# Optimization experiments

Hardware: AMD Instinct MI355X
Metric: run time of the kernel (lower is better)

Reference implementation:

```python
import jax, jax.numpy as jnp
import numpy as np

D_MODEL = 1024
N_EXPERTS = 16
TOP_K = 2
EXPERT_DIM = 1024
SHARED_DIM = 2048
B, T = 2, 1024


def setup_inputs() -> dict:
    key = jax.random.key(0)
    ks = jax.random.split(key, 7)
    std = 0.02
    return {
        "x": jax.random.normal(ks[0], (B, T, D_MODEL), dtype=jnp.float32),
        "router_w": jax.random.normal(ks[1], (N_EXPERTS, D_MODEL), dtype=jnp.float32) * std,
        "gate_up_w": jax.random.normal(ks[2], (N_EXPERTS, D_MODEL, 2 * EXPERT_DIM), dtype=jnp.float32) * std,
        "down_w": jax.random.normal(ks[3], (N_EXPERTS, EXPERT_DIM, D_MODEL), dtype=jnp.float32) * std,
        "shared_gate_w": jax.random.normal(ks[4], (SHARED_DIM, D_MODEL), dtype=jnp.float32) * std,
        "shared_up_w": jax.random.normal(ks[5], (SHARED_DIM, D_MODEL), dtype=jnp.float32) * std,
        "shared_down_w": jax.random.normal(ks[6], (D_MODEL, SHARED_DIM), dtype=jnp.float32) * std,
    }


def reference(x, router_w, gate_up_w, down_w, shared_gate_w, shared_up_w, shared_down_w):
    Bb, Tt, C = x.shape
    N = Bb * Tt
    E = gate_up_w.shape[0]

    # Router: top-k logits, sigmoid gating (matches torch.topk then sigmoid).
    logits = jnp.einsum('btc,ec->bte', x, router_w)          # [B,T,E]
    top_vals, top_idx = jax.lax.top_k(logits, TOP_K)          # [B,T,K]
    gates = jax.nn.sigmoid(top_vals)

    xf = x.reshape(N, C)
    sel = top_idx.reshape(N, TOP_K)
    gw = gates.reshape(N, TOP_K)

    # Dense per-token expert gate [N,E]: zero except selected experts.
    # top_k indices are distinct per token, so scatter-add == scatter-set.
    w_full = jnp.zeros((N, E), dtype=x.dtype).at[jnp.arange(N)[:, None], sel].add(gw)

    # Run every token through every expert densely (same math as the
    # per-token gather + bmm + scatter_add combine, without materializing
    # [N*K, C, 2H] gathered weight tensors).
    gu = jnp.einsum('nc,ech->neh', xf, gate_up_w)             # [N,E,2H]
    gate, up = jnp.split(gu, 2, axis=-1)
    h = jax.nn.silu(gate) * up                                # [N,E,H]
    out_all = jnp.einsum('neh,ehc->nec', h, down_w)           # [N,E,C]
    moe = jnp.einsum('ne,nec->nc', w_full, out_all).reshape(Bb, Tt, C)

    # Shared expert (SwiGLU MLP).
    sg = jnp.einsum('btc,sc->bts', x, shared_gate_w)
    su = jnp.einsum('btc,sc->bts', x, shared_up_w)
    shared = jnp.einsum('bts,cs->btc', jax.nn.silu(sg) * su, shared_down_w)

    return moe + shared
```

## Files before the change

kernel.cpp:

```cpp
#include <hip/hip_runtime.h>
#include <cstdint>

#define N_TOK 2048
#define CDIM  1024
#define NEXP  16
#define TOPK  2
#define HDIM  1024
#define SDIM  2048
#define ESLOT 48
#define ESLOT64 80
#define GU_EXP_BLOCKS (ESLOT * 16)
#define GU_SH_BLOCKS  (16 * 32)
#define GU_NWG (GU_EXP_BLOCKS + GU_SH_BLOCKS)
#define DN_EXP_BLOCKS (ESLOT64 * 8)
#define DN_SH_BLOCKS  (32 * 8)
#define DN_NWG (DN_EXP_BLOCKS + DN_SH_BLOCKS)

typedef __bf16 bf16;
typedef __bf16 bf16x8 __attribute__((ext_vector_type(8)));
typedef float  f32x4  __attribute__((ext_vector_type(4)));
typedef unsigned int u32;
typedef unsigned short u16;

typedef __attribute__((address_space(3))) uint32_t lds_u32_t;
typedef __attribute__((address_space(1))) uint32_t glb_u32_t;

__device__ __forceinline__ void gload16(const void* g, void* l) {
  __builtin_amdgcn_global_load_lds((const glb_u32_t*)(uintptr_t)g,
                                   (lds_u32_t*)(uintptr_t)l, 16, 0, 0);
}
__device__ __forceinline__ float fromb(u16 s) {
  union { float f; u32 u; } z; z.u = ((u32)s) << 16; return z.f;
}
__device__ __forceinline__ int xcd_swz(int bid, int nwg) {
  return (bid & 7) * (nwg >> 3) + (bid >> 3);
}
#define SBAR0() __builtin_amdgcn_sched_barrier(0)
#define WAIT_VM(N) do { asm volatile("s_waitcnt vmcnt(" #N ")" ::: "memory"); \
                        SBAR0(); } while (0)

__global__ void convert_plain(const float* __restrict__ s, bf16* __restrict__ d) {
  int i = (blockIdx.x * 256 + threadIdx.x) * 8;
  float4 f0 = *(const float4*)(s + i);
  float4 f1 = *(const float4*)(s + i + 4);
  bf16x8 v;
  v[0]=(bf16)f0.x; v[1]=(bf16)f0.y; v[2]=(bf16)f0.z; v[3]=(bf16)f0.w;
  v[4]=(bf16)f1.x; v[5]=(bf16)f1.y; v[6]=(bf16)f1.z; v[7]=(bf16)f1.w;
  *(bf16x8*)(d + i) = v;
}

__global__ __launch_bounds__(256)
void convert_t(const float* __restrict__ src, bf16* __restrict__ dst, int K, int N) {
  __shared__ float ld[64 * 68];
  const int e = blockIdx.z;
  const int n0 = blockIdx.x * 64, k0 = blockIdx.y * 64;
  const float* s = src + (size_t)e * K * N;
  bf16* d = dst + (size_t)e * N * K;
  const int t = threadIdx.x;
  const int kk = t >> 4, c4 = (t & 15) * 4;
#pragma unroll
  for (int q = 0; q < 4; ++q) {
    float4 f = *(const float4*)(s + (size_t)(k0 + kk + q * 16) * N + n0 + c4);
    float* lp = &ld[(kk + q * 16) * 68 + c4];
    lp[0] = f.x; lp[1] = f.y; lp[2] = f.z; lp[3] = f.w;
  }
  __syncthreads();
  const int nn = t >> 2, kc = (t & 3) * 16;
  bf16x8 v0, v1;
#pragma unroll
  for (int j = 0; j < 8; ++j) {
    v0[j] = (bf16)ld[(kc + j) * 68 + nn];
    v1[j] = (bf16)ld[(kc + 8 + j) * 68 + nn];
  }
  bf16* dp = d + (size_t)(n0 + nn) * K + k0 + kc;
  *(bf16x8*)dp = v0;
  *(bf16x8*)(dp + 8) = v1;
}

__global__ void router_kernel(const float* __restrict__ x,
                              const float* __restrict__ rw,
                              bf16* __restrict__ xb,
                              int* __restrict__ sel,
                              float* __restrict__ gatew) {
  int n = blockIdx.x;
  int lane = threadIdx.x;
  const float* xr = x + (size_t)n * CDIM;
  float xv[16];
#pragma unroll
  for (int q = 0; q < 4; ++q) {
    float4 f = *(const float4*)(xr + lane * 16 + q * 4);
    xv[q * 4 + 0] = f.x; xv[q * 4 + 1] = f.y; xv[q * 4 + 2] = f.z; xv[q * 4 + 3] = f.w;
  }
  bf16x8 v0, v1;
#pragma unroll
  for (int j = 0; j < 8; ++j) { v0[j] = (bf16)xv[j]; v1[j] = (bf16)xv[8 + j]; }
  bf16* xo = xb + (size_t)n * CDIM + lane * 16;
  *(bf16x8*)xo = v0;
  *(bf16x8*)(xo + 8) = v1;
  float acc[NEXP];
#pragma unroll
  for (int e = 0; e < NEXP; ++e) {
    float a = 0.f;
    const float* rwe = rw + e * CDIM + lane * 16;
#pragma unroll
    for (int j = 0; j < 16; ++j) a += xv[j] * rwe[j];
    acc[e] = a;
  }
#pragma unroll
  for (int off = 32; off > 0; off >>= 1) {
#pragma unroll
    for (int e = 0; e < NEXP; ++e) acc[e] += __shfl_xor(acc[e], off, 64);
  }
  if (lane == 0) {
    int i0 = 0; float v0_ = acc[0];
#pragma unroll
    for (int e = 1; e < NEXP; ++e) if (acc[e] > v0_) { v0_ = acc[e]; i0 = e; }
    int i1 = (i0 == 0) ? 1 : 0; float v1_ = acc[i1];
#pragma unroll
    for (int e = 0; e < NEXP; ++e) if (e != i0 && acc[e] > v1_) { v1_ = acc[e]; i1 = e; }
    sel[2 * n] = i0; sel[2 * n + 1] = i1;
    gatew[2 * n]     = 1.f / (1.f + expf(-v0_));
    gatew[2 * n + 1] = 1.f / (1.f + expf(-v1_));
  }
}

__global__ void scan_kernel(const int* __restrict__ sel,
                            int* __restrict__ counts,
                            int* __restrict__ offsets,
                            int* __restrict__ cursor,
                            int* __restrict__ tab128,
                            int* __restrict__ tab64,
                            int* __restrict__ ntiles) {
  __shared__ int hist[NEXP];
  const int t = threadIdx.x;
  if (t < NEXP) hist[t] = 0;
  __syncthreads();
  for (int i = t; i < N_TOK * TOPK; i += 256) atomicAdd(&hist[sel[i]], 1);
  __syncthreads();
  if (t == 0) {
    int s = 0, a = 0, b = 0;
    for (int e = 0; e < NEXP; ++e) {
      int c = hist[e];
      counts[e] = c; offsets[e] = s; cursor[e] = s;
      for (int m0 = 0; m0 < c; m0 += 128) tab128[a++] = (e << 16) | m0;
      for (int m0 = 0; m0 < c; m0 += 64)  tab64[b++]  = (e << 16) | m0;
      s += c;
    }
    ntiles[0] = a; ntiles[1] = b;
  }
}

__global__ void scatter_kernel(const int* __restrict__ sel,
                               const float* __restrict__ gatew,
                               int* __restrict__ cursor,
                               int* __restrict__ entry_token,
                               float* __restrict__ entry_gate,
                               int* __restrict__ entry_pos) {
  int t = blockIdx.x * blockDim.x + threadIdx.x;
  if (t >= N_TOK * TOPK) return;
  int e = sel[t];
  int pos = atomicAdd(&cursor[e], 1);
  entry_token[pos] = t >> 1;
  entry_gate[pos] = gatew[t];
  entry_pos[t] = pos;
}

__global__ __launch_bounds__(256, 2)
void gu7(const bf16* __restrict__ xb,
         const bf16* __restrict__ guwb,
         const bf16* __restrict__ sgwb,
         const bf16* __restrict__ suwb,
         bf16* __restrict__ h_exp,
         bf16* __restrict__ h_sh,
         const int* __restrict__ counts,
         const int* __restrict__ offsets,
         const int* __restrict__ entry_token,
         const int* __restrict__ tab128,
         const int* __restrict__ ntiles) {
  __shared__ __align__(16) bf16 sA[2 * 8192];
  __shared__ __align__(16) bf16 sBg[3 * 4096];
  __shared__ __align__(16) bf16 sBu[3 * 4096];

  const int bid = xcd_swz(blockIdx.x, GU_NWG);
  const int t = threadIdx.x;
  const bool is_exp = bid < GU_EXP_BLOCKS;
  const int wid = t >> 6, lane = t & 63;

  int n0, mguard;
  bf16* hbase; int hstride;
  const bf16 *Bg, *Bu;
  const int srow = t >> 3;
  const int sc = (t & 7) ^ (srow & 7);
  const bf16* asrc[4];

  if (is_exp) {
    const int slot = bid >> 4;
    if (slot >= ntiles[0]) return;
    const int packed = tab128[slot];
    const int e = packed >> 16;
    const int m0 = packed & 0xffff;
    const int cnt = counts[e];
    const int base = offsets[e];
    n0 = (bid & 15) * 64;
    mguard = cnt - m0;
#pragma unroll
    for (int i = 0; i < 4; ++i) {
      int r = m0 + i * 32 + srow;
      int tok = entry_token[base + ((r < cnt) ? r : (cnt - 1))];
      asrc[i] = xb + (size_t)tok * CDIM + sc * 8;
    }
    const bf16* we = guwb + (size_t)e * (2 * HDIM) * CDIM;
    Bg = we + (size_t)n0 * CDIM;
    Bu = we + (size_t)(HDIM + n0) * CDIM;
    hbase = h_exp + (size_t)(base + m0) * HDIM + n0;
    hstride = HDIM;
  } else {
    const int sid = bid - GU_EXP_BLOCKS;
    const int m0 = (sid >> 5) * 128;
    n0 = (sid & 31) * 64;
    mguard = 128;
#pragma unroll
    for (int i = 0; i < 4; ++i)
      asrc[i] = xb + (size_t)(m0 + i * 32 + srow) * CDIM + sc * 8;
    Bg = sgwb + (size_t)n0 * CDIM;
    Bu = suwb + (size_t)n0 * CDIM;
    hbase = h_sh + (size_t)m0 * SDIM + n0;
    hstride = SDIM;
  }

  const bf16* bg0 = Bg + (size_t)srow * CDIM + sc * 8;
  const bf16* bu0 = Bu + (size_t)srow * CDIM + sc * 8;
  const int adst = t * 8;

#define ISSUE_A(k_, ab_)                                                      \
  do {                                                                        \
    _Pragma("unroll")                                                         \
    for (int i = 0; i < 4; ++i)                                               \
      gload16(asrc[i] + (k_), &sA[(ab_) * 8192 + adst + i * 2048]);           \
  } while (0)
#define ISSUE_B(k_, bo_)                                                      \
  do {                                                                        \
    _Pragma("unroll")                                                         \
    for (int i = 0; i < 2; ++i) {                                             \
      gload16(bg0 + (size_t)i * 32 * CDIM + (k_), &sBg[(bo_) + adst + i * 2048]); \
      gload16(bu0 + (size_t)i * 32 * CDIM + (k_), &sBu[(bo_) + adst + i * 2048]); \
    }                                                                         \
  } while (0)

  const int wr = (wid >> 1) * 64, wc = (wid & 1) * 32;
  const int lrow = lane & 15, grp = lane >> 4;

  f32x4 ag[4][2], au[4][2];
#pragma unroll
  for (int m = 0; m < 4; ++m)
#pragma unroll
    for (int n = 0; n < 2; ++n)
#pragma unroll
      for (int i = 0; i < 4; ++i) { ag[m][n][i] = 0.f; au[m][n][i] = 0.f; }

#define COMPUTE(ab_, bo_)                                                     \
  do {                                                                        \
    _Pragma("unroll")                                                         \
    for (int ks = 0; ks < 2; ++ks) {                                          \
      const int ch = ks * 4 + grp;                                            \
      bf16x8 av[4], bg[2], bu[2];                                             \
      _Pragma("unroll")                                                       \
      for (int m = 0; m < 4; ++m) {                                           \
        const int r = wr + m * 16 + lrow;                                     \
        av[m] = *(const bf16x8*)&sA[(ab_) * 8192 + r * 64 + ((ch ^ (r & 7)) << 3)]; \
      }                                                                       \
      _Pragma("unroll")                                                       \
      for (int n = 0; n < 2; ++n) {                                           \
        const int r = wc + n * 16 + lrow;                                     \
        bg[n] = *(const bf16x8*)&sBg[(bo_) + r * 64 + ((ch ^ (r & 7)) << 3)]; \
        bu[n] = *(const bf16x8*)&sBu[(bo_) + r * 64 + ((ch ^ (r & 7)) << 3)]; \
      }                                                                       \
      _Pragma("unroll")                                                       \
      for (int m = 0; m < 4; ++m)                                             \
        _Pragma("unroll")                                                     \
        for (int n = 0; n < 2; ++n) {                                         \
          ag[m][n] = __builtin_amdgcn_mfma_f32_16x16x32_bf16(av[m], bg[n], ag[m][n], 0, 0, 0); \
          au[m][n] = __builtin_amdgcn_mfma_f32_16x16x32_bf16(av[m], bu[n], au[m][n], 0, 0, 0); \
        }                                                                     \
    }                                                                         \
  } while (0)

  ISSUE_A(0, 0);
  ISSUE_B(0, 0);
  SBAR0();
  ISSUE_B(64, 4096);
  SBAR0();
  WAIT_VM(4);
  __builtin_amdgcn_s_barrier();

  int bb0 = 0, bb1 = 4096, bb2 = 8192;
  for (int k = 0; k < 14; ++k) {
    ISSUE_A((k + 1) * 64, (k + 1) & 1);
    SBAR0();
    ISSUE_B((k + 2) * 64, bb2);
    SBAR0();
    COMPUTE(k & 1, bb0);
    WAIT_VM(4);
    __builtin_amdgcn_s_barrier();
    int tmp = bb0; bb0 = bb1; bb1 = bb2; bb2 = tmp;
  }
  ISSUE_A(15 * 64, 1);
  SBAR0();
  COMPUTE(0, bb0);
  WAIT_VM(0);
  __builtin_amdgcn_s_barrier();
  { int tmp = bb0; bb0 = bb1; bb1 = bb2; bb2 = tmp; }
  COMPUTE(1, bb0);
#undef ISSUE_A
#undef ISSUE_B
#undef COMPUTE

#pragma unroll
  for (int m = 0; m < 4; ++m) {
#pragma unroll
    for (int i = 0; i < 4; ++i) {
      const int rl = wr + m * 16 + grp * 4 + i;
      if (rl >= mguard) continue;
      bf16* orow = hbase + (size_t)rl * hstride;
#pragma unroll
      for (int n = 0; n < 2; ++n) {
        const float g = ag[m][n][i];
        const float u = au[m][n][i];
        orow[wc + n * 16 + lrow] = (bf16)(g * u * __builtin_amdgcn_rcpf(1.f + __expf(-g)));
      }
    }
  }
}

__global__ __launch_bounds__(256, 2)
void dn7(const bf16* __restrict__ h_exp,
         const bf16* __restrict__ h_sh,
         const bf16* __restrict__ dwb,
         const bf16* __restrict__ sdwb,
         const float* __restrict__ entry_gate,
         bf16* __restrict__ out_e,
         float* __restrict__ out,
         const int* __restrict__ counts,
         const int* __restrict__ offsets,
         const int* __restrict__ tab64,
         const int* __restrict__ ntiles) {
  __shared__ __align__(16) bf16 sA[2 * 4096];
  __shared__ __align__(16) bf16 sB[3 * 8192];

  const int bid = xcd_swz(blockIdx.x, DN_NWG);
  const int t = threadIdx.x;
  const bool is_exp = bid < DN_EXP_BLOCKS;
  const int wid = t >> 6, lane = t & 63;

  int n0, mguard, K, rowbase, NK;
  const bf16* Ab;
  const bf16* Bb;

  if (is_exp) {
    const int slot = bid >> 3;
    if (slot >= ntiles[1]) return;
    const int packed = tab64[slot];
    const int e = packed >> 16;
    const int m0 = packed & 0xffff;
    const int cnt = counts[e];
    n0 = (bid & 7) * 128;
    mguard = cnt - m0;
    K = HDIM; NK = HDIM / 64;
    rowbase = offsets[e] + m0;
    Ab = h_exp;
    Bb = dwb + (size_t)e * CDIM * HDIM + (size_t)n0 * HDIM;
  } else {
    const int sid = bid - DN_EXP_BLOCKS;
    const int m0 = (sid >> 3) * 64;
    n0 = (sid & 7) * 128;
    mguard = 64;
    K = SDIM; NK = SDIM / 64;
    rowbase = m0;
    Ab = h_sh;
    Bb = sdwb + (size_t)n0 * SDIM;
  }

  const int srow = t >> 3;
  const int sc = (t & 7) ^ (srow & 7);
  const bf16* asrc[2];
#pragma unroll
  for (int i = 0; i < 2; ++i) {
    int rg = rowbase + i * 32 + srow;
    if (is_exp && rg > N_TOK * TOPK - 1) rg = N_TOK * TOPK - 1;
    asrc[i] = Ab + (size_t)rg * K + sc * 8;
  }
  const bf16* b0 = Bb + (size_t)srow * K + sc * 8;
  const int adst = t * 8;

#define ISSUE_A(k_, ab_)                                                      \
  do {                                                                        \
    _Pragma("unroll")                                                         \
    for (int i = 0; i < 2; ++i)                                               \
      gload16(asrc[i] + (k_), &sA[(ab_) * 4096 + adst + i * 2048]);           \
  } while (0)
#define ISSUE_B(k_, bo_)                                                      \
  do {                                                                        \
    _Pragma("unroll")                                                         \
    for (int i = 0; i < 4; ++i)                                               \
      gload16(b0 + (size_t)i * 32 * K + (k_), &sB[(bo_) + adst + i * 2048]);  \
  } while (0)

  const int wr = (wid >> 1) * 32, wc = (wid & 1) * 64;
  const int lrow = lane & 15, grp = lane >> 4;

  f32x4 acc[2][4];
#pragma unroll
  for (int m = 0; m < 2; ++m)
#pragma unroll
    for (int n = 0; n < 4; ++n)
#pragma unroll
      for (int i = 0; i < 4; ++i) acc[m][n][i] = 0.f;

#define COMPUTE(ab_, bo_)                                                     \
  do {                                                                        \
    _Pragma("unroll")                                                         \
    for (int ks = 0; ks < 2; ++ks) {                                          \
      const int ch = ks * 4 + grp;                                            \
      bf16x8 av[2], bv[4];                                                    \
      _Pragma("unroll")                                                       \
      for (int m = 0; m < 2; ++m) {                                           \
        const int r = wr + m * 16 + lrow;                                     \
        av[m] = *(const bf16x8*)&sA[(ab_) * 4096 + r * 64 + ((ch ^ (r & 7)) << 3)]; \
      }                                                                       \
      _Pragma("unroll")                                                       \
      for (int n = 0; n < 4; ++n) {                                           \
        const int r = wc + n * 16 + lrow;                                     \
        bv[n] = *(const bf16x8*)&sB[(bo_) + r * 64 + ((ch ^ (r & 7)) << 3)];  \
      }                                                                       \
      _Pragma("unroll")                                                       \
      for (int m = 0; m < 2; ++m)                                             \
        _Pragma("unroll")                                                     \
        for (int n = 0; n < 4; ++n)                                           \
          acc[m][n] = __builtin_amdgcn_mfma_f32_16x16x32_bf16(av[m], bv[n], acc[m][n], 0, 0, 0); \
    }                                                                         \
  } while (0)

  ISSUE_A(0, 0);
  ISSUE_B(0, 0);
  SBAR0();
  ISSUE_B(64, 8192);
  SBAR0();
  WAIT_VM(4);
  __builtin_amdgcn_s_barrier();

  int bb0 = 0, bb1 = 8192, bb2 = 16384;
  for (int k = 0; k < NK - 2; ++k) {
    ISSUE_A((k + 1) * 64, (k + 1) & 1);
    SBAR0();
    ISSUE_B((k + 2) * 64, bb2);
    SBAR0();
    COMPUTE(k & 1, bb0);
    WAIT_VM(4);
    __builtin_amdgcn_s_barrier();
    int tmp = bb0; bb0 = bb1; bb1 = bb2; bb2 = tmp;
  }
  ISSUE_A((NK - 1) * 64, (NK - 1) & 1);
  SBAR0();
  COMPUTE((NK - 2) & 1, bb0);
  WAIT_VM(0);
  __builtin_amdgcn_s_barrier();
  { int tmp = bb0; bb0 = bb1; bb1 = bb2; bb2 = tmp; }
  COMPUTE((NK - 1) & 1, bb0);
#undef ISSUE_A
#undef ISSUE_B
#undef COMPUTE

#pragma unroll
  for (int m = 0; m < 2; ++m) {
#pragma unroll
    for (int i = 0; i < 4; ++i) {
      const int rl = wr + m * 16 + grp * 4 + i;
      if (rl >= mguard) continue;
      if (is_exp) {
        const int row = rowbase + rl;
        const float scl = entry_gate[row];
        bf16* orow = out_e + (size_t)row * CDIM + n0;
#pragma unroll
        for (int n = 0; n < 4; ++n)
          orow[wc + n * 16 + lrow] = (bf16)(acc[m][n][i] * scl);
      } else {
        float* orow = out + (size_t)(rowbase + rl) * CDIM + n0;
#pragma unroll
        for (int n = 0; n < 4; ++n)
          orow[wc + n * 16 + lrow] = acc[m][n][i];
      }
    }
  }
}

__global__ void combine_kernel(float* __restrict__ out,
                               const bf16* __restrict__ out_e,
                               const int* __restrict__ entry_pos) {
  int tid = blockIdx.x * blockDim.x + threadIdx.x;
  int n = tid >> 8;
  int c4 = tid & 255;
  int p0 = entry_pos[2 * n];
  int p1 = entry_pos[2 * n + 1];
  float4 v = ((const float4*)out)[tid];
  ushort4 a = *(const ushort4*)((const u16*)out_e + (size_t)p0 * CDIM + c4 * 4);
  ushort4 b = *(const ushort4*)((const u16*)out_e + (size_t)p1 * CDIM + c4 * 4);
  v.x += fromb(a.x) + fromb(b.x);
  v.y += fromb(a.y) + fromb(b.y);
  v.z += fromb(a.z) + fromb(b.z);
  v.w += fromb(a.w) + fromb(b.w);
  ((float4*)out)[tid] = v;
}

extern "C" void kernel_launch(void* const* d_in, const int* in_sizes, int n_in,
                              void* d_out, int out_size, void* d_ws, size_t ws_size,
                              hipStream_t stream) {
  const float* x   = (const float*)d_in[0];
  const float* rw  = (const float*)d_in[1];
  const float* guw = (const float*)d_in[2];
  const float* dw  = (const float*)d_in[3];
  const float* sgw = (const float*)d_in[4];
  const float* suw = (const float*)d_in[5];
  const float* sdw = (const float*)d_in[6];
  float* out = (float*)d_out;
  char* ws = (char*)d_ws;
  const size_t MB = 1048576;

  int*   sel         = (int*)(ws + 0);
  float* gatew       = (float*)(ws + 16384);
  int*   counts      = (int*)(ws + 32768);
  int*   offsets     = (int*)(ws + 32832);
  int*   cursor      = (int*)(ws + 32896);
  int*   ntiles      = (int*)(ws + 32960);
  int*   tab128      = (int*)(ws + 33024);
  int*   tab64       = (int*)(ws + 33280);
  int*   entry_token = (int*)(ws + 33664);
  float* entry_gate  = (float*)(ws + 50048);
  int*   entry_pos   = (int*)(ws + 66432);

  bf16* xb    = (bf16*)(ws + 82816);
  bf16* h_exp = (bf16*)(ws + 82816 + 4 * MB);
  bf16* h_sh  = (bf16*)(ws + 82816 + 12 * MB);
  bf16* sgw_b = (bf16*)(ws + 82816 + 20 * MB);
  bf16* suw_b = (bf16*)(ws + 82816 + 24 * MB);
  bf16* Wbig  = (bf16*)(ws + 82816 + 28 * MB);
  bf16* out_e = sgw_b;
  bf16* sdw_b = xb;

  router_kernel<<<N_TOK, 64, 0, stream>>>(x, rw, xb, sel, gatew);
  scan_kernel<<<1, 256, 0, stream>>>(sel, counts, offsets, cursor, tab128, tab64, ntiles);
  scatter_kernel<<<16, 256, 0, stream>>>(sel, gatew, cursor, entry_token, entry_gate, entry_pos);

  convert_t<<<dim3(32, 16, NEXP), 256, 0, stream>>>(guw, Wbig, CDIM, 2 * HDIM);
  convert_plain<<<1024, 256, 0, stream>>>(sgw, sgw_b);
  convert_plain<<<1024, 256, 0, stream>>>(suw, suw_b);

  gu7<<<GU_NWG, 256, 0, stream>>>(xb, Wbig, sgw_b, suw_b, h_exp, h_sh,
                                  counts, offsets, entry_token, tab128, ntiles);

  convert_t<<<dim3(16, 16, NEXP), 256, 0, stream>>>(dw, Wbig, HDIM, CDIM);
  convert_plain<<<1024, 256, 0, stream>>>(sdw, sdw_b);

  dn7<<<DN_NWG, 256, 0, stream>>>(h_exp, h_sh, Wbig, sdw_b, entry_gate, out_e, out,
                                  counts, offsets, tab64, ntiles);

  combine_kernel<<<(N_TOK * CDIM / 4) / 256, 256, 0, stream>>>(out, out_e, entry_pos);
}
```

Baseline: 192.1 us.

## Halve GEMM K-tile to 32, raise occupancy to 4, fuse scan/scatter and converts

Both grouped GEMM kernels now stage K-tiles of 32 instead of 64. That halves LDS per block, so launch bounds can ask for 4 workgroups per CU, and the LDS swizzle is reworked to fit the narrower rows. The scan and scatter kernels are merged into one single-block kernel that uses an LDS cursor. The three shared-weight conversions become one launch, with sdw_b moved to its own buffer so it can be converted early. The cost is twice as many barrier and wait iterations with less MFMA work per stage, and possible register pressure at the higher occupancy target.

Result: slower. 202.6 us (+5.4%).

```diff
diff --git a/kernel.cpp b/kernel.cpp
--- a/kernel.cpp
+++ b/kernel.cpp
@@ -39,8 +39,18 @@
 #define WAIT_VM(N) do { asm volatile("s_waitcnt vmcnt(" #N ")" ::: "memory"); \
                         SBAR0(); } while (0)
 
-__global__ void convert_plain(const float* __restrict__ s, bf16* __restrict__ d) {
-  int i = (blockIdx.x * 256 + threadIdx.x) * 8;
+__global__ void convert_small3(const float* __restrict__ sgw,
+                               const float* __restrict__ suw,
+                               const float* __restrict__ sdw,
+                               bf16* __restrict__ sgw_b,
+                               bf16* __restrict__ suw_b,
+                               bf16* __restrict__ sdw_b) {
+  const int b = blockIdx.x;
+  const float* s; bf16* d;
+  if (b < 1024)       { s = sgw; d = sgw_b; }
+  else if (b < 2048)  { s = suw; d = suw_b; }
+  else                { s = sdw; d = sdw_b; }
+  int i = ((b & 1023) * 256 + threadIdx.x) * 8;
   float4 f0 = *(const float4*)(s + i);
   float4 f1 = *(const float4*)(s + i + 4);
   bf16x8 v;
@@ -124,14 +134,17 @@
   }
 }
 
-__global__ void scan_kernel(const int* __restrict__ sel,
-                            int* __restrict__ counts,
-                            int* __restrict__ offsets,
-                            int* __restrict__ cursor,
-                            int* __restrict__ tab128,
-                            int* __restrict__ tab64,
-                            int* __restrict__ ntiles) {
-  __shared__ int hist[NEXP];
+__global__ void scan_scatter(const int* __restrict__ sel,
+                             const float* __restrict__ gatew,
+                             int* __restrict__ counts,
+                             int* __restrict__ offsets,
+                             int* __restrict__ tab128,
+                             int* __restrict__ tab64,
+                             int* __restrict__ ntiles,
+                             int* __restrict__ entry_token,
+                             float* __restrict__ entry_gate,
+                             int* __restrict__ entry_pos) {
+  __shared__ int hist[NEXP], cur[NEXP];
   const int t = threadIdx.x;
   if (t < NEXP) hist[t] = 0;
   __syncthreads();
@@ -141,32 +154,25 @@
     int s = 0, a = 0, b = 0;
     for (int e = 0; e < NEXP; ++e) {
       int c = hist[e];
-      counts[e] = c; offsets[e] = s; cursor[e] = s;
+      counts[e] = c; offsets[e] = s; cur[e] = s;
       for (int m0 = 0; m0 < c; m0 += 128) tab128[a++] = (e << 16) | m0;
       for (int m0 = 0; m0 < c; m0 += 64)  tab64[b++]  = (e << 16) | m0;
       s += c;
     }
     ntiles[0] = a; ntiles[1] = b;
   }
-}
-
-__global__ void scatter_kernel(const int* __restrict__ sel,
-                               const float* __restrict__ gatew,
-                               int* __restrict__ cursor,
-                               int* __restrict__ entry_token,
-                               float* __restrict__ entry_gate,
-                               int* __restrict__ entry_pos) {
-  int t = blockIdx.x * blockDim.x + threadIdx.x;
-  if (t >= N_TOK * TOPK) return;
-  int e = sel[t];
-  int pos = atomicAdd(&cursor[e], 1);
-  entry_token[pos] = t >> 1;
-  entry_gate[pos] = gatew[t];
-  entry_pos[t] = pos;
-}
-
-__global__ __launch_bounds__(256, 2)
-void gu7(const bf16* __restrict__ xb,
+  __syncthreads();
+  for (int i = t; i < N_TOK * TOPK; i += 256) {
+    int e = sel[i];
+    int pos = atomicAdd(&cur[e], 1);
+    entry_token[pos] = i >> 1;
+    entry_gate[pos] = gatew[i];
+    entry_pos[i] = pos;
+  }
+}
+
+__global__ __launch_bounds__(256, 4)
+void gu8(const bf16* __restrict__ xb,
          const bf16* __restrict__ guwb,
          const bf16* __restrict__ sgwb,
          const bf16* __restrict__ suwb,
@@ -177,9 +183,9 @@
          const int* __restrict__ entry_token,
          const int* __restrict__ tab128,
          const int* __restrict__ ntiles) {
-  __shared__ __align__(16) bf16 sA[2 * 8192];
-  __shared__ __align__(16) bf16 sBg[3 * 4096];
-  __shared__ __align__(16) bf16 sBu[3 * 4096];
+  __shared__ __align__(16) bf16 sA[2 * 4096];
+  __shared__ __align__(16) bf16 sBg[3 * 2048];
+  __shared__ __align__(16) bf16 sBu[3 * 2048];
 
   const int bid = xcd_swz(blockIdx.x, GU_NWG);
   const int t = threadIdx.x;
@@ -189,9 +195,9 @@
   int n0, mguard;
   bf16* hbase; int hstride;
   const bf16 *Bg, *Bu;
-  const int srow = t >> 3;
-  const int sc = (t & 7) ^ (srow & 7);
-  const bf16* asrc[4];
+  const int prow = t >> 2;
+  const int ppos = t & 3;
+  const bf16* asrc[2];
 
   if (is_exp) {
     const int slot = bid >> 4;
@@ -204,10 +210,12 @@
     n0 = (bid & 15) * 64;
     mguard = cnt - m0;
 #pragma unroll
-    for (int i = 0; i < 4; ++i) {
-      int r = m0 + i * 32 + srow;
+    for (int i = 0; i < 2; ++i) {
+      const int row = i * 64 + prow;
+      int r = m0 + row;
       int tok = entry_token[base + ((r < cnt) ? r : (cnt - 1))];
-      asrc[i] = xb + (size_t)tok * CDIM + sc * 8;
+      const int c = ppos ^ ((row >> 1) & 3);
+      asrc[i] = xb + (size_t)tok * CDIM + c * 8;
     }
     const bf16* we = guwb + (size_t)e * (2 * HDIM) * CDIM;
     Bg = we + (size_t)n0 * CDIM;
@@ -220,31 +228,32 @@
     n0 = (sid & 31) * 64;
     mguard = 128;
 #pragma unroll
-    for (int i = 0; i < 4; ++i)
-      asrc[i] = xb + (size_t)(m0 + i * 32 + srow) * CDIM + sc * 8;
+    for (int i = 0; i < 2; ++i) {
+      const int row = i * 64 + prow;
+      const int c = ppos ^ ((row >> 1) & 3);
+      asrc[i] = xb + (size_t)(m0 + row) * CDIM + c * 8;
+    }
     Bg = sgwb + (size_t)n0 * CDIM;
     Bu = suwb + (size_t)n0 * CDIM;
     hbase = h_sh + (size_t)m0 * SDIM + n0;
     hstride = SDIM;
   }
 
-  const bf16* bg0 = Bg + (size_t)srow * CDIM + sc * 8;
-  const bf16* bu0 = Bu + (size_t)srow * CDIM + sc * 8;
-  const int adst = t * 8;
+  const int bc = ppos ^ ((prow >> 1) & 3);
+  const bf16* bg0 = Bg + (size_t)prow * CDIM + bc * 8;
+  const bf16* bu0 = Bu + (size_t)prow * CDIM + bc * 8;
+  const int pdst = t * 8;
 
 #define ISSUE_A(k_, ab_)                                                      \
   do {                                                                        \
     _Pragma("unroll")                                                         \
-    for (int i = 0; i < 4; ++i)                                               \
-      gload16(asrc[i] + (k_), &sA[(ab_) * 8192 + adst + i * 2048]);           \
+    for (int i = 0; i < 2; ++i)                                               \
+      gload16(asrc[i] + (k_), &sA[(ab_) * 4096 + i * 2048 + pdst]);           \
   } while (0)
 #define ISSUE_B(k_, bo_)                                                      \
   do {                                                                        \
-    _Pragma("unroll")                                                         \
-    for (int i = 0; i < 2; ++i) {                                             \
-      gload16(bg0 + (size_t)i * 32 * CDIM + (k_), &sBg[(bo_) + adst + i * 2048]); \
-      gload16(bu0 + (size_t)i * 32 * CDIM + (k_), &sBu[(bo_) + adst + i * 2048]); \
-    }                                                                         \
+    gload16(bg0 + (k_), &sBg[(bo_) + pdst]);                                  \
+    gload16(bu0 + (k_), &sBu[(bo_) + pdst]);                                  \
   } while (0)
 
   const int wr = (wid >> 1) * 64, wc = (wid & 1) * 32;
@@ -260,51 +269,49 @@
 
 #define COMPUTE(ab_, bo_)                                                     \
   do {                                                                        \
-    _Pragma("unroll")                                                         \
-    for (int ks = 0; ks < 2; ++ks) {                                          \
-      const int ch = ks * 4 + grp;                                            \
-      bf16x8 av[4], bg[2], bu[2];                                             \
-      _Pragma("unroll")                                                       \
-      for (int m = 0; m < 4; ++m) {                                           \
-        const int r = wr + m * 16 + lrow;                                     \
-        av[m] = *(const bf16x8*)&sA[(ab_) * 8192 + r * 64 + ((ch ^ (r & 7)) << 3)]; \
-      }                                                                       \
+    bf16x8 av[4], bg[2], bu[2];                                               \
+    _Pragma("unroll")                                                         \
+    for (int m = 0; m < 4; ++m) {                                             \
+      const int r = wr + m * 16 + lrow;                                       \
+      av[m] = *(const bf16x8*)&sA[(ab_) * 4096 + r * 32 +                     \
+                                  ((grp ^ ((r >> 1) & 3)) << 3)];             \
+    }                                                                         \
+    _Pragma("unroll")                                                         \
+    for (int n = 0; n < 2; ++n) {                                             \
+      const int r = wc + n * 16 + lrow;                                       \
+      const int so = r * 32 + ((grp ^ ((r >> 1) & 3)) << 3);                  \
+      bg[n] = *(const bf16x8*)&sBg[(bo_) + so];                               \
+      bu[n] = *(const bf16x8*)&sBu[(bo_) + so];                               \
+    }                                                                         \
+    _Pragma("unroll")                                                         \
+    for (int m = 0; m < 4; ++m)                                               \
       _Pragma("unroll")                                                       \
       for (int n = 0; n < 2; ++n) {                                           \
-        const int r = wc + n * 16 + lrow;                                     \
-        bg[n] = *(const bf16x8*)&sBg[(bo_) + r * 64 + ((ch ^ (r & 7)) << 3)]; \
-        bu[n] = *(const bf16x8*)&sBu[(bo_) + r * 64 + ((ch ^ (r & 7)) << 3)]; \
+        ag[m][n] = __builtin_amdgcn_mfma_f32_16x16x32_bf16(av[m], bg[n], ag[m][n], 0, 0, 0); \
+        au[m][n] = __builtin_amdgcn_mfma_f32_16x16x32_bf16(av[m], bu[n], au[m][n], 0, 0, 0); \
       }                                                                       \
-      _Pragma("unroll")                                                       \
-      for (int m = 0; m < 4; ++m)                                             \
-        _Pragma("unroll")                                                     \
-        for (int n = 0; n < 2; ++n) {                                         \
-          ag[m][n] = __builtin_amdgcn_mfma_f32_16x16x32_bf16(av[m], bg[n], ag[m][n], 0, 0, 0); \
-          au[m][n] = __builtin_amdgcn_mfma_f32_16x16x32_bf16(av[m], bu[n], au[m][n], 0, 0, 0); \
-        }                                                                     \
-    }                                                                         \
   } while (0)
 
   ISSUE_A(0, 0);
   ISSUE_B(0, 0);
   SBAR0();
-  ISSUE_B(64, 4096);
+  ISSUE_B(32, 2048);
   SBAR0();
-  WAIT_VM(4);
+  WAIT_VM(2);
   __builtin_amdgcn_s_barrier();
 
-  int bb0 = 0, bb1 = 4096, bb2 = 8192;
-  for (int k = 0; k < 14; ++k) {
-    ISSUE_A((k + 1) * 64, (k + 1) & 1);
+  int bb0 = 0, bb1 = 2048, bb2 = 4096;
+  for (int k = 0; k < 30; ++k) {
+    ISSUE_A((k + 1) * 32, (k + 1) & 1);
     SBAR0();
-    ISSUE_B((k + 2) * 64, bb2);
+    ISSUE_B((k + 2) * 32, bb2);
     SBAR0();
     COMPUTE(k & 1, bb0);
-    WAIT_VM(4);
+    WAIT_VM(2);
     __builtin_amdgcn_s_barrier();
     int tmp = bb0; bb0 = bb1; bb1 = bb2; bb2 = tmp;
   }
-  ISSUE_A(15 * 64, 1);
+  ISSUE_A(31 * 32, 1);
   SBAR0();
   COMPUTE(0, bb0);
   WAIT_VM(0);
@@ -332,8 +339,8 @@
   }
 }
 
-__global__ __launch_bounds__(256, 2)
-void dn7(const bf16* __restrict__ h_exp,
+__global__ __launch_bounds__(256, 4)
+void dn8(const bf16* __restrict__ h_exp,
          const bf16* __restrict__ h_sh,
          const bf16* __restrict__ dwb,
          const bf16* __restrict__ sdwb,
@@ -344,8 +351,8 @@
          const int* __restrict__ offsets,
          const int* __restrict__ tab64,
          const int* __restrict__ ntiles) {
-  __shared__ __align__(16) bf16 sA[2 * 4096];
-  __shared__ __align__(16) bf16 sB[3 * 8192];
+  __shared__ __align__(16) bf16 sA[2 * 2048];
+  __shared__ __align__(16) bf16 sB[3 * 4096];
 
   const int bid = xcd_swz(blockIdx.x, DN_NWG);
   const int t = threadIdx.x;
@@ -365,7 +372,7 @@
     const int cnt = counts[e];
     n0 = (bid & 7) * 128;
     mguard = cnt - m0;
-    K = HDIM; NK = HDIM / 64;
+    K = HDIM; NK = HDIM / 32;
     rowbase = offsets[e] + m0;
     Ab = h_exp;
     Bb = dwb + (size_t)e * CDIM * HDIM + (size_t)n0 * HDIM;
@@ -374,35 +381,34 @@
     const int m0 = (sid >> 3) * 64;
     n0 = (sid & 7) * 128;
     mguard = 64;
-    K = SDIM; NK = SDIM / 64;
+    K = SDIM; NK = SDIM / 32;
     rowbase = m0;
     Ab = h_sh;
     Bb = sdwb + (size_t)n0 * SDIM;
   }
 
-  const int srow = t >> 3;
-  const int sc = (t & 7) ^ (srow & 7);
-  const bf16* asrc[2];
+  const int prow = t >> 2;
+  const int ppos = t & 3;
+  int arg = rowbase + prow;
+  if (is_exp && arg > N_TOK * TOPK - 1) arg = N_TOK * TOPK - 1;
+  const int ac = ppos ^ ((prow >> 1) & 3);
+  const bf16* asrc = Ab + (size_t)arg * K + ac * 8;
+  const bf16* bsrc[2];
 #pragma unroll
   for (int i = 0; i < 2; ++i) {
-    int rg = rowbase + i * 32 + srow;
-    if (is_exp && rg > N_TOK * TOPK - 1) rg = N_TOK * TOPK - 1;
-    asrc[i] = Ab + (size_t)rg * K + sc * 8;
-  }
-  const bf16* b0 = Bb + (size_t)srow * K + sc * 8;
-  const int adst = t * 8;
+    const int row = i * 64 + prow;
+    const int c = ppos ^ ((row >> 1) & 3);
+    bsrc[i] = Bb + (size_t)row * K + c * 8;
+  }
+  const int pdst = t * 8;
 
 #define ISSUE_A(k_, ab_)                                                      \
-  do {                                                                        \
-    _Pragma("unroll")                                                         \
-    for (int i = 0; i < 2; ++i)                                               \
-      gload16(asrc[i] + (k_), &sA[(ab_) * 4096 + adst + i * 2048]);           \
-  } while (0)
+  gload16(asrc + (k_), &sA[(ab_) * 2048 + pdst])
 #define ISSUE_B(k_, bo_)                                                      \
   do {                                                                        \
     _Pragma("unroll")                                                         \
-    for (int i = 0; i < 4; ++i)                                               \
-      gload16(b0 + (size_t)i * 32 * K + (k_), &sB[(bo_) + adst + i * 2048]);  \
+    for (int i = 0; i < 2; ++i)                                               \
+      gload16(bsrc[i] + (k_), &sB[(bo_) + i * 2048 + pdst]);                  \
   } while (0)
 
   const int wr = (wid >> 1) * 32, wc = (wid & 1) * 64;
@@ -418,48 +424,46 @@
 
 #define COMPUTE(ab_, bo_)                                                     \
   do {                                                                        \
-    _Pragma("unroll")                                                         \
-    for (int ks = 0; ks < 2; ++ks) {                                          \
-      const int ch = ks * 4 + grp;                                            \
-      bf16x8 av[2], bv[4];                                                    \
+    bf16x8 av[2], bv[4];                                                      \
+    _Pragma("unroll")                                                         \
+    for (int m = 0; m < 2; ++m) {                                             \
+      const int r = wr + m * 16 + lrow;                                       \
+      av[m] = *(const bf16x8*)&sA[(ab_) * 2048 + r * 32 +                     \
+                                  ((grp ^ ((r >> 1) & 3)) << 3)];             \
+    }                                                                         \
+    _Pragma("unroll")                                                         \
+    for (int n = 0; n < 4; ++n) {                                             \
+      const int r = wc + n * 16 + lrow;                                       \
+      bv[n] = *(const bf16x8*)&sB[(bo_) + r * 32 +                            \
+                                  ((grp ^ ((r >> 1) & 3)) << 3)];             \
+    }                                                                         \
+    _Pragma("unroll")                                                         \
+    for (int m = 0; m < 2; ++m)                                               \
       _Pragma("unroll")                                                       \
-      for (int m = 0; m < 2; ++m) {                                           \
-        const int r = wr + m * 16 + lrow;                                     \
-        av[m] = *(const bf16x8*)&sA[(ab_) * 4096 + r * 64 + ((ch ^ (r & 7)) << 3)]; \
-      }                                                                       \
-      _Pragma("unroll")                                                       \
-      for (int n = 0; n < 4; ++n) {                                           \
-        const int r = wc + n * 16 + lrow;                                     \
-        bv[n] = *(const bf16x8*)&sB[(bo_) + r * 64 + ((ch ^ (r & 7)) << 3)];  \
-      }                                                                       \
-      _Pragma("unroll")                                                       \
-      for (int m = 0; m < 2; ++m)                                             \
-        _Pragma("unroll")                                                     \
-        for (int n = 0; n < 4; ++n)                                           \
-          acc[m][n] = __builtin_amdgcn_mfma_f32_16x16x32_bf16(av[m], bv[n], acc[m][n], 0, 0, 0); \
-    }                                                                         \
+      for (int n = 0; n < 4; ++n)                                             \
+        acc[m][n] = __builtin_amdgcn_mfma_f32_16x16x32_bf16(av[m], bv[n], acc[m][n], 0, 0, 0); \
   } while (0)
 
   ISSUE_A(0, 0);
   ISSUE_B(0, 0);
   SBAR0();
-  ISSUE_B(64, 8192);
+  ISSUE_B(32, 4096);
   SBAR0();
-  WAIT_VM(4);
+  WAIT_VM(2);
   __builtin_amdgcn_s_barrier();
 
-  int bb0 = 0, bb1 = 8192, bb2 = 16384;
+  int bb0 = 0, bb1 = 4096, bb2 = 8192;
   for (int k = 0; k < NK - 2; ++k) {
-    ISSUE_A((k + 1) * 64, (k + 1) & 1);
+    ISSUE_A((k + 1) * 32, (k + 1) & 1);
     SBAR0();
-    ISSUE_B((k + 2) * 64, bb2);
+    ISSUE_B((k + 2) * 32, bb2);
     SBAR0();
     COMPUTE(k & 1, bb0);
-    WAIT_VM(4);
+    WAIT_VM(2);
     __builtin_amdgcn_s_barrier();
     int tmp = bb0; bb0 = bb1; bb1 = bb2; bb2 = tmp;
   }
-  ISSUE_A((NK - 1) * 64, (NK - 1) & 1);
+  ISSUE_A((NK - 1) * 32, (NK - 1) & 1);
   SBAR0();
   COMPUTE((NK - 2) & 1, bb0);
   WAIT_VM(0);
@@ -529,7 +533,6 @@
   float* gatew       = (float*)(ws + 16384);
   int*   counts      = (int*)(ws + 32768);
   int*   offsets     = (int*)(ws + 32832);
-  int*   cursor      = (int*)(ws + 32896);
   int*   ntiles      = (int*)(ws + 32960);
   int*   tab128      = (int*)(ws + 33024);
   int*   tab64       = (int*)(ws + 33280);
@@ -543,24 +546,22 @@
   bf16* sgw_b = (bf16*)(ws + 82816 + 20 * MB);
   bf16* suw_b = (bf16*)(ws + 82816 + 24 * MB);
   bf16* Wbig  = (bf16*)(ws + 82816 + 28 * MB);
+  bf16* sdw_b = (bf16*)(ws + 82816 + 92 * MB);
   bf16* out_e = sgw_b;
-  bf16* sdw_b = xb;
 
   router_kernel<<<N_TOK, 64, 0, stream>>>(x, rw, xb, sel, gatew);
-  scan_kernel<<<1, 256, 0, stream>>>(sel, counts, offsets, cursor, tab128, tab64, ntiles);
-  scatter_kernel<<<16, 256, 0, stream>>>(sel, gatew, cursor, entry_token, entry_gate, entry_pos);
+  scan_scatter<<<1, 256, 0, stream>>>(sel, gatew, counts, offsets, tab128, tab64,
+                                      ntiles, entry_token, entry_gate, entry_pos);
 
   convert_t<<<dim3(32, 16, NEXP), 256, 0, stream>>>(guw, Wbig, CDIM, 2 * HDIM);
-  convert_plain<<<1024, 256, 0, stream>>>(sgw, sgw_b);
-  convert_plain<<<1024, 256, 0, stream>>>(suw, suw_b);
-
-  gu7<<<GU_NWG, 256, 0, stream>>>(xb, Wbig, sgw_b, suw_b, h_exp, h_sh,
+  convert_small3<<<3072, 256, 0, stream>>>(sgw, suw, sdw, sgw_b, suw_b, sdw_b);
+
+  gu8<<<GU_NWG, 256, 0, stream>>>(xb, Wbig, sgw_b, suw_b, h_exp, h_sh,
                                   counts, offsets, entry_token, tab128, ntiles);
 
   convert_t<<<dim3(16, 16, NEXP), 256, 0, stream>>>(dw, Wbig, HDIM, CDIM);
-  convert_plain<<<1024, 256, 0, stream>>>(sdw, sdw_b);
-
-  dn7<<<DN_NWG, 256, 0, stream>>>(h_exp, h_sh, Wbig, sdw_b, entry_gate, out_e, out,
+
+  dn8<<<DN_NWG, 256, 0, stream>>>(h_exp, h_sh, Wbig, sdw_b, entry_gate, out_e, out,
                                   counts, offsets, tab64, ntiles);
 
   combine_kernel<<<(N_TOK * CDIM / 4) / 256, 256, 0, stream>>>(out, out_e, entry_pos);
```

## Use 512-thread blocks for MoE GEMMs and merge small setup kernels

Applied to the files above, without the earlier changes.

Both the gate/up and down GEMM kernels now run with 512 threads per block (8 waves) instead of 256. Each wave computes a smaller output sub-tile, and the down kernel's M tile grows from 64 to 128 rows so it shares the 128-row tile table. The scan and scatter kernels are merged into a single block that uses LDS cursors, and the three shared-weight conversions are merged into one launch. This cuts launch count and redistributes load/compute across more waves, at the cost of more padding waste on partial 128-row expert tiles and possibly different occupancy.

After: 178.0 us. -7.4%, faster.

```diff
diff --git a/kernel.cpp b/kernel.cpp
--- a/kernel.cpp
+++ b/kernel.cpp
@@ -8,12 +8,11 @@
 #define HDIM  1024
 #define SDIM  2048
 #define ESLOT 48
-#define ESLOT64 80
 #define GU_EXP_BLOCKS (ESLOT * 16)
 #define GU_SH_BLOCKS  (16 * 32)
 #define GU_NWG (GU_EXP_BLOCKS + GU_SH_BLOCKS)
-#define DN_EXP_BLOCKS (ESLOT64 * 8)
-#define DN_SH_BLOCKS  (32 * 8)
+#define DN_EXP_BLOCKS (ESLOT * 8)
+#define DN_SH_BLOCKS  (16 * 8)
 #define DN_NWG (DN_EXP_BLOCKS + DN_SH_BLOCKS)
 
 typedef __bf16 bf16;
@@ -39,8 +38,18 @@
 #define WAIT_VM(N) do { asm volatile("s_waitcnt vmcnt(" #N ")" ::: "memory"); \
                         SBAR0(); } while (0)
 
-__global__ void convert_plain(const float* __restrict__ s, bf16* __restrict__ d) {
-  int i = (blockIdx.x * 256 + threadIdx.x) * 8;
+__global__ void convert_small3(const float* __restrict__ sgw,
+                               const float* __restrict__ suw,
+                               const float* __restrict__ sdw,
+                               bf16* __restrict__ sgw_b,
+                               bf16* __restrict__ suw_b,
+                               bf16* __restrict__ sdw_b) {
+  const int b = blockIdx.x;
+  const float* s; bf16* d;
+  if (b < 1024)       { s = sgw; d = sgw_b; }
+  else if (b < 2048)  { s = suw; d = suw_b; }
+  else                { s = sdw; d = sdw_b; }
+  int i = ((b & 1023) * 256 + threadIdx.x) * 8;
   float4 f0 = *(const float4*)(s + i);
   float4 f1 = *(const float4*)(s + i + 4);
   bf16x8 v;
@@ -124,49 +133,43 @@
   }
 }
 
-__global__ void scan_kernel(const int* __restrict__ sel,
-                            int* __restrict__ counts,
-                            int* __restrict__ offsets,
-                            int* __restrict__ cursor,
-                            int* __restrict__ tab128,
-                            int* __restrict__ tab64,
-                            int* __restrict__ ntiles) {
-  __shared__ int hist[NEXP];
+__global__ void scan_scatter(const int* __restrict__ sel,
+                             const float* __restrict__ gatew,
+                             int* __restrict__ counts,
+                             int* __restrict__ offsets,
+                             int* __restrict__ tab128,
+                             int* __restrict__ ntiles,
+                             int* __restrict__ entry_token,
+                             float* __restrict__ entry_gate,
+                             int* __restrict__ entry_pos) {
+  __shared__ int hist[NEXP], cur[NEXP];
   const int t = threadIdx.x;
   if (t < NEXP) hist[t] = 0;
   __syncthreads();
   for (int i = t; i < N_TOK * TOPK; i += 256) atomicAdd(&hist[sel[i]], 1);
   __syncthreads();
   if (t == 0) {
-    int s = 0, a = 0, b = 0;
+    int s = 0, a = 0;
     for (int e = 0; e < NEXP; ++e) {
       int c = hist[e];
-      counts[e] = c; offsets[e] = s; cursor[e] = s;
+      counts[e] = c; offsets[e] = s; cur[e] = s;
       for (int m0 = 0; m0 < c; m0 += 128) tab128[a++] = (e << 16) | m0;
-      for (int m0 = 0; m0 < c; m0 += 64)  tab64[b++]  = (e << 16) | m0;
       s += c;
     }
-    ntiles[0] = a; ntiles[1] = b;
-  }
-}
-
-__global__ void scatter_kernel(const int* __restrict__ sel,
-                               const float* __restrict__ gatew,
-                               int* __restrict__ cursor,
-                               int* __restrict__ entry_token,
-                               float* __restrict__ entry_gate,
-                               int* __restrict__ entry_pos) {
-  int t = blockIdx.x * blockDim.x + threadIdx.x;
-  if (t >= N_TOK * TOPK) return;
-  int e = sel[t];
-  int pos = atomicAdd(&cursor[e], 1);
-  entry_token[pos] = t >> 1;
-  entry_gate[pos] = gatew[t];
-  entry_pos[t] = pos;
-}
-
-__global__ __launch_bounds__(256, 2)
-void gu7(const bf16* __restrict__ xb,
+    ntiles[0] = a;
+  }
+  __syncthreads();
+  for (int i = t; i < N_TOK * TOPK; i += 256) {
+    int e = sel[i];
+    int pos = atomicAdd(&cur[e], 1);
+    entry_token[pos] = i >> 1;
+    entry_gate[pos] = gatew[i];
+    entry_pos[i] = pos;
+  }
+}
+
+__global__ __launch_bounds__(512, 2)
+void gu9(const bf16* __restrict__ xb,
          const bf16* __restrict__ guwb,
          const bf16* __restrict__ sgwb,
          const bf16* __restrict__ suwb,
@@ -189,9 +192,9 @@
   int n0, mguard;
   bf16* hbase; int hstride;
   const bf16 *Bg, *Bu;
-  const int srow = t >> 3;
-  const int sc = (t & 7) ^ (srow & 7);
-  const bf16* asrc[4];
+  const int arow = t >> 3;
+  const int sc = (t & 7) ^ (arow & 7);
+  const bf16* asrc[2];
 
   if (is_exp) {
     const int slot = bid >> 4;
@@ -204,8 +207,8 @@
     n0 = (bid & 15) * 64;
     mguard = cnt - m0;
 #pragma unroll
-    for (int i = 0; i < 4; ++i) {
-      int r = m0 + i * 32 + srow;
+    for (int i = 0; i < 2; ++i) {
+      int r = m0 + i * 64 + arow;
       int tok = entry_token[base + ((r < cnt) ? r : (cnt - 1))];
       asrc[i] = xb + (size_t)tok * CDIM + sc * 8;
     }
@@ -220,39 +223,46 @@
     n0 = (sid & 31) * 64;
     mguard = 128;
 #pragma unroll
-    for (int i = 0; i < 4; ++i)
-      asrc[i] = xb + (size_t)(m0 + i * 32 + srow) * CDIM + sc * 8;
+    for (int i = 0; i < 2; ++i)
+      asrc[i] = xb + (size_t)(m0 + i * 64 + arow) * CDIM + sc * 8;
     Bg = sgwb + (size_t)n0 * CDIM;
     Bu = suwb + (size_t)n0 * CDIM;
     hbase = h_sh + (size_t)m0 * SDIM + n0;
     hstride = SDIM;
   }
 
-  const bf16* bg0 = Bg + (size_t)srow * CDIM + sc * 8;
-  const bf16* bu0 = Bu + (size_t)srow * CDIM + sc * 8;
+  const int th = t & 255;
+  bf16* bdst = (t >= 256) ? sBu : sBg;
+  const bf16* Bp = (t >= 256) ? Bu : Bg;
+  const bf16* bsrc[2];
+#pragma unroll
+  for (int i = 0; i < 2; ++i) {
+    const int row = i * 32 + (th >> 3);
+    const int c = (th & 7) ^ (row & 7);
+    bsrc[i] = Bp + (size_t)row * CDIM + c * 8;
+  }
   const int adst = t * 8;
+  const int bdoff = th * 8;
 
 #define ISSUE_A(k_, ab_)                                                      \
   do {                                                                        \
     _Pragma("unroll")                                                         \
-    for (int i = 0; i < 4; ++i)                                               \
-      gload16(asrc[i] + (k_), &sA[(ab_) * 8192 + adst + i * 2048]);           \
+    for (int i = 0; i < 2; ++i)                                               \
+      gload16(asrc[i] + (k_), &sA[(ab_) * 8192 + i * 4096 + adst]);           \
   } while (0)
 #define ISSUE_B(k_, bo_)                                                      \
   do {                                                                        \
     _Pragma("unroll")                                                         \
-    for (int i = 0; i < 2; ++i) {                                             \
-      gload16(bg0 + (size_t)i * 32 * CDIM + (k_), &sBg[(bo_) + adst + i * 2048]); \
-      gload16(bu0 + (size_t)i * 32 * CDIM + (k_), &sBu[(bo_) + adst + i * 2048]); \
-    }                                                                         \
+    for (int i = 0; i < 2; ++i)                                               \
+      gload16(bsrc[i] + (k_), &bdst[(bo_) + i * 2048 + bdoff]);               \
   } while (0)
 
-  const int wr = (wid >> 1) * 64, wc = (wid & 1) * 32;
+  const int wr = (wid >> 1) * 32, wc = (wid & 1) * 32;
   const int lrow = lane & 15, grp = lane >> 4;
 
-  f32x4 ag[4][2], au[4][2];
-#pragma unroll
-  for (int m = 0; m < 4; ++m)
+  f32x4 ag[2][2], au[2][2];
+#pragma unroll
+  for (int m = 0; m < 2; ++m)
 #pragma unroll
     for (int n = 0; n < 2; ++n)
 #pragma unroll
@@ -263,20 +273,21 @@
     _Pragma("unroll")                                                         \
     for (int ks = 0; ks < 2; ++ks) {                                          \
       const int ch = ks * 4 + grp;                                            \
-      bf16x8 av[4], bg[2], bu[2];                                             \
+      bf16x8 av[2], bg[2], bu[2];                                             \
       _Pragma("unroll")                                                       \
-      for (int m = 0; m < 4; ++m) {                                           \
+      for (int m = 0; m < 2; ++m) {                                           \
         const int r = wr + m * 16 + lrow;                                     \
         av[m] = *(const bf16x8*)&sA[(ab_) * 8192 + r * 64 + ((ch ^ (r & 7)) << 3)]; \
       }                                                                       \
       _Pragma("unroll")                                                       \
       for (int n = 0; n < 2; ++n) {                                           \
         const int r = wc + n * 16 + lrow;                                     \
-        bg[n] = *(const bf16x8*)&sBg[(bo_) + r * 64 + ((ch ^ (r & 7)) << 3)]; \
-        bu[n] = *(const bf16x8*)&sBu[(bo_) + r * 64 + ((ch ^ (r & 7)) << 3)]; \
+        const int so = r * 64 + ((ch ^ (r & 7)) << 3);                        \
+        bg[n] = *(const bf16x8*)&sBg[(bo_) + so];                             \
+        bu[n] = *(const bf16x8*)&sBu[(bo_) + so];                             \
       }                                                                       \
       _Pragma("unroll")                                                       \
-      for (int m = 0; m < 4; ++m)                                             \
+      for (int m = 0; m < 2; ++m)                                             \
         _Pragma("unroll")                                                     \
         for (int n = 0; n < 2; ++n) {                                         \
           ag[m][n] = __builtin_amdgcn_mfma_f32_16x16x32_bf16(av[m], bg[n], ag[m][n], 0, 0, 0); \
@@ -290,7 +301,7 @@
   SBAR0();
   ISSUE_B(64, 4096);
   SBAR0();
-  WAIT_VM(4);
+  WAIT_VM(2);
   __builtin_amdgcn_s_barrier();
 
   int bb0 = 0, bb1 = 4096, bb2 = 8192;
@@ -300,7 +311,7 @@
     ISSUE_B((k + 2) * 64, bb2);
     SBAR0();
     COMPUTE(k & 1, bb0);
-    WAIT_VM(4);
+    WAIT_VM(2);
     __builtin_amdgcn_s_barrier();
     int tmp = bb0; bb0 = bb1; bb1 = bb2; bb2 = tmp;
   }
@@ -316,7 +327,7 @@
 #undef COMPUTE
 
 #pragma unroll
-  for (int m = 0; m < 4; ++m) {
+  for (int m = 0; m < 2; ++m) {
 #pragma unroll
     for (int i = 0; i < 4; ++i) {
       const int rl = wr + m * 16 + grp * 4 + i;
@@ -332,8 +343,8 @@
   }
 }
 
-__global__ __launch_bounds__(256, 2)
-void dn7(const bf16* __restrict__ h_exp,
+__global__ __launch_bounds__(512, 2)
+void dn9(const bf16* __restrict__ h_exp,
          const bf16* __restrict__ h_sh,
          const bf16* __restrict__ dwb,
          const bf16* __restrict__ sdwb,
@@ -342,9 +353,9 @@
          float* __restrict__ out,
          const int* __restrict__ counts,
          const int* __restrict__ offsets,
-         const int* __restrict__ tab64,
+         const int* __restrict__ tab128,
          const int* __restrict__ ntiles) {
-  __shared__ __align__(16) bf16 sA[2 * 4096];
+  __shared__ __align__(16) bf16 sA[2 * 8192];
   __shared__ __align__(16) bf16 sB[3 * 8192];
 
   const int bid = xcd_swz(blockIdx.x, DN_NWG);
@@ -358,8 +369,8 @@
 
   if (is_exp) {
     const int slot = bid >> 3;
-    if (slot >= ntiles[1]) return;
-    const int packed = tab64[slot];
+    if (slot >= ntiles[0]) return;
+    const int packed = tab128[slot];
     const int e = packed >> 16;
     const int m0 = packed & 0xffff;
     const int cnt = counts[e];
@@ -371,38 +382,41 @@
     Bb = dwb + (size_t)e * CDIM * HDIM + (size_t)n0 * HDIM;
   } else {
     const int sid = bid - DN_EXP_BLOCKS;
-    const int m0 = (sid >> 3) * 64;
+    const int m0 = (sid >> 3) * 128;
     n0 = (sid & 7) * 128;
-    mguard = 64;
+    mguard = 128;
     K = SDIM; NK = SDIM / 64;
     rowbase = m0;
     Ab = h_sh;
     Bb = sdwb + (size_t)n0 * SDIM;
   }
 
-  const int srow = t >> 3;
-  const int sc = (t & 7) ^ (srow & 7);
+  const int arow = t >> 3;
+  const int sc = (t & 7) ^ (arow & 7);
   const bf16* asrc[2];
 #pragma unroll
   for (int i = 0; i < 2; ++i) {
-    int rg = rowbase + i * 32 + srow;
+    int rg = rowbase + i * 64 + arow;
     if (is_exp && rg > N_TOK * TOPK - 1) rg = N_TOK * TOPK - 1;
     asrc[i] = Ab + (size_t)rg * K + sc * 8;
   }
-  const bf16* b0 = Bb + (size_t)srow * K + sc * 8;
+  const bf16* bsrc[2];
+#pragma unroll
+  for (int i = 0; i < 2; ++i)
+    bsrc[i] = Bb + (size_t)(i * 64 + arow) * K + sc * 8;
   const int adst = t * 8;
 
 #define ISSUE_A(k_, ab_)                                                      \
   do {                                                                        \
     _Pragma("unroll")                                                         \
     for (int i = 0; i < 2; ++i)                                               \
-      gload16(asrc[i] + (k_), &sA[(ab_) * 4096 + adst + i * 2048]);           \
+      gload16(asrc[i] + (k_), &sA[(ab_) * 8192 + i * 4096 + adst]);           \
   } while (0)
 #define ISSUE_B(k_, bo_)                                                      \
   do {                                                                        \
     _Pragma("unroll")                                                         \
-    for (int i = 0; i < 4; ++i)                                               \
-      gload16(b0 + (size_t)i * 32 * K + (k_), &sB[(bo_) + adst + i * 2048]);  \
+    for (int i = 0; i < 2; ++i)                                               \
+      gload16(bsrc[i] + (k_), &sB[(bo_) + i * 4096 + adst]);                  \
   } while (0)
 
   const int wr = (wid >> 1) * 32, wc = (wid & 1) * 64;
@@ -425,7 +439,7 @@
       _Pragma("unroll")                                                       \
       for (int m = 0; m < 2; ++m) {                                           \
         const int r = wr + m * 16 + lrow;                                     \
-        av[m] = *(const bf16x8*)&sA[(ab_) * 4096 + r * 64 + ((ch ^ (r & 7)) << 3)]; \
+        av[m] = *(const bf16x8*)&sA[(ab_) * 8192 + r * 64 + ((ch ^ (r & 7)) << 3)]; \
       }                                                                       \
       _Pragma("unroll")                                                       \
       for (int n = 0; n < 4; ++n) {                                           \
@@ -445,7 +459,7 @@
   SBAR0();
   ISSUE_B(64, 8192);
   SBAR0();
-  WAIT_VM(4);
+  WAIT_VM(2);
   __builtin_amdgcn_s_barrier();
 
   int bb0 = 0, bb1 = 8192, bb2 = 16384;
@@ -455,7 +469,7 @@
     ISSUE_B((k + 2) * 64, bb2);
     SBAR0();
     COMPUTE(k & 1, bb0);
-    WAIT_VM(4);
+    WAIT_VM(2);
     __builtin_amdgcn_s_barrier();
     int tmp = bb0; bb0 = bb1; bb1 = bb2; bb2 = tmp;
   }
@@ -529,10 +543,8 @@
   float* gatew       = (float*)(ws + 16384);
   int*   counts      = (int*)(ws + 32768);
   int*   offsets     = (int*)(ws + 32832);
-  int*   cursor      = (int*)(ws + 32896);
   int*   ntiles      = (int*)(ws + 32960);
   int*   tab128      = (int*)(ws + 33024);
-  int*   tab64       = (int*)(ws + 33280);
   int*   entry_token = (int*)(ws + 33664);
   float* entry_gate  = (float*)(ws + 50048);
   int*   entry_pos   = (int*)(ws + 66432);
@@ -543,25 +555,23 @@
   bf16* sgw_b = (bf16*)(ws + 82816 + 20 * MB);
   bf16* suw_b = (bf16*)(ws + 82816 + 24 * MB);
   bf16* Wbig  = (bf16*)(ws + 82816 + 28 * MB);
+  bf16* sdw_b = (bf16*)(ws + 82816 + 92 * MB);
   bf16* out_e = sgw_b;
-  bf16* sdw_b = xb;
 
   router_kernel<<<N_TOK, 64, 0, stream>>>(x, rw, xb, sel, gatew);
-  scan_kernel<<<1, 256, 0, stream>>>(sel, counts, offsets, cursor, tab128, tab64, ntiles);
-  scatter_kernel<<<16, 256, 0, stream>>>(sel, gatew, cursor, entry_token, entry_gate, entry_pos);
+  scan_scatter<<<1, 256, 0, stream>>>(sel, gatew, counts, offsets, tab128,
+                                      ntiles, entry_token, entry_gate, entry_pos);
 
   convert_t<<<dim3(32, 16, NEXP), 256, 0, stream>>>(guw, Wbig, CDIM, 2 * HDIM);
-  convert_plain<<<1024, 256, 0, stream>>>(sgw, sgw_b);
-  convert_plain<<<1024, 256, 0, stream>>>(suw, suw_b);
-
-  gu7<<<GU_NWG, 256, 0, stream>>>(xb, Wbig, sgw_b, suw_b, h_exp, h_sh,
+  convert_small3<<<3072, 256, 0, stream>>>(sgw, suw, sdw, sgw_b, suw_b, sdw_b);
+
+  gu9<<<GU_NWG, 512, 0, stream>>>(xb, Wbig, sgw_b, suw_b, h_exp, h_sh,
                                   counts, offsets, entry_token, tab128, ntiles);
 
   convert_t<<<dim3(16, 16, NEXP), 256, 0, stream>>>(dw, Wbig, HDIM, CDIM);
-  convert_plain<<<1024, 256, 0, stream>>>(sdw, sdw_b);
-
-  dn7<<<DN_NWG, 256, 0, stream>>>(h_exp, h_sh, Wbig, sdw_b, entry_gate, out_e, out,
-                                  counts, offsets, tab64, ntiles);
+
+  dn9<<<DN_NWG, 512, 0, stream>>>(h_exp, h_sh, Wbig, sdw_b, entry_gate, out_e, out,
+                                  counts, offsets, tab128, ntiles);
 
   combine_kernel<<<(N_TOK * CDIM / 4) / 256, 256, 0, stream>>>(out, out_e, entry_pos);
 }
```
